# Optimization experiments

Hardware: AMD Instinct MI355X
Metric: run time of the kernel (lower is better)

## Reference

```python
import jax, jax.numpy as jnp
import numpy as np

N_NODES = 50000
N_EDGES = 800000
IN_C = 128
HID = 128
OUT_C = 64
N_GRAPHS = 256


def setup_inputs() -> dict:
    key = jax.random.key(0)
    ks = jax.random.split(key, 12)
    x = jax.random.normal(ks[0], (N_NODES, IN_C), dtype=jnp.float32)
    edge_index = jax.random.randint(ks[1], (2, N_EDGES), 0, N_NODES, dtype=jnp.int32)
    batch = jnp.sort(jax.random.randint(ks[2], (N_NODES,), 0, N_GRAPHS, dtype=jnp.int32))
    def lin(k, fan_in, fan_out):
        bound = 1.0 / np.sqrt(fan_in)
        kw, kb = jax.random.split(k)
        W = jax.random.uniform(kw, (fan_in, fan_out), minval=-bound, maxval=bound, dtype=jnp.float32)
        b = jax.random.uniform(kb, (fan_out,), minval=-bound, maxval=bound, dtype=jnp.float32)
        return W, b
    W1a, b1a = lin(ks[3], IN_C, HID)
    W1b, b1b = lin(ks[4], HID, HID)
    W2a, b2a = lin(ks[5], HID, HID)
    W2b, b2b = lin(ks[6], HID, HID)
    Wl, bl = lin(ks[7], HID, OUT_C)
    return {"x": x, "edge_index": edge_index, "batch": batch,
            "W1a": W1a, "b1a": b1a, "W1b": W1b, "b1b": b1b,
            "W2a": W2a, "b2a": b2a, "W2b": W2b, "b2b": b2b,
            "Wl": Wl, "bl": bl}


def gin_conv(x, edge_index, Wa, ba, Wb, bb):
    # GINConv with eps=0: h_i = MLP(x_i + sum_{j->i} x_j)
    src, dst = edge_index[0], edge_index[1]
    agg = jax.ops.segment_sum(x[src], dst, num_segments=x.shape[0])  # [N, d]
    h = x + agg
    h = jax.nn.relu(h @ Wa + ba) @ Wb + bb
    return h


def reference(x, edge_index, batch, W1a, b1a, W1b, b1b, W2a, b2a, W2b, b2b, Wl, bl):
    h = gin_conv(x, edge_index, W1a, b1a, W1b, b1b)
    h = gin_conv(h, edge_index, W2a, b2a, W2b, b2b)
    # global mean pool over graphs in the batch
    sums = jax.ops.segment_sum(h, batch, num_segments=N_GRAPHS)          # [G, HID]
    cnts = jax.ops.segment_sum(jnp.ones((h.shape[0],), h.dtype), batch, num_segments=N_GRAPHS)
    pooled = sums / jnp.maximum(cnts, 1.0)[:, None]
    return pooled @ Wl + bl  # [G, OUT_C]
```

## Files before the change

kernel.cpp:

```cpp
#include <hip/hip_runtime.h>

constexpr int N  = 50000;
constexpr int E  = 800000;
constexpr int C  = 128;
constexpr int G  = 256;
constexpr int OC = 64;
constexpr int D  = 64;

constexpr int TB = (E / 4 + 255) / 256;
constexpr int WB = 256;
constexpr int XB = (N * C / 8 + 255) / 256;

typedef __attribute__((ext_vector_type(8))) short short8;
typedef __attribute__((ext_vector_type(4))) float f32x4;
typedef __attribute__((ext_vector_type(2))) float f32x2;

__device__ __forceinline__ unsigned int au(float f) { return __float_as_uint(f); }

__device__ __forceinline__ unsigned short f2bf(float f) {
    unsigned int u = au(f);
    u += 0x7fffu + ((u >> 16) & 1u);
    return (unsigned short)(u >> 16);
}
__device__ __forceinline__ unsigned int pack_bf16(float lo, float hi) {
    return ((au(hi) + 0x8000u) & 0xFFFF0000u) | ((au(lo) + 0x8000u) >> 16);
}

__device__ __forceinline__ void acc16(f32x2* a, uint4 v) {
    a[0] += __builtin_amdgcn_cvt_pk_f32_fp8((int)v.x, false);
    a[1] += __builtin_amdgcn_cvt_pk_f32_fp8((int)v.x, true);
    a[2] += __builtin_amdgcn_cvt_pk_f32_fp8((int)v.y, false);
    a[3] += __builtin_amdgcn_cvt_pk_f32_fp8((int)v.y, true);
    a[4] += __builtin_amdgcn_cvt_pk_f32_fp8((int)v.z, false);
    a[5] += __builtin_amdgcn_cvt_pk_f32_fp8((int)v.z, true);
    a[6] += __builtin_amdgcn_cvt_pk_f32_fp8((int)v.w, false);
    a[7] += __builtin_amdgcn_cvt_pk_f32_fp8((int)v.w, true);
}
__device__ __forceinline__ void set16(f32x2* a, uint4 v) {
    a[0] = __builtin_amdgcn_cvt_pk_f32_fp8((int)v.x, false);
    a[1] = __builtin_amdgcn_cvt_pk_f32_fp8((int)v.x, true);
    a[2] = __builtin_amdgcn_cvt_pk_f32_fp8((int)v.y, false);
    a[3] = __builtin_amdgcn_cvt_pk_f32_fp8((int)v.y, true);
    a[4] = __builtin_amdgcn_cvt_pk_f32_fp8((int)v.z, false);
    a[5] = __builtin_amdgcn_cvt_pk_f32_fp8((int)v.z, true);
    a[6] = __builtin_amdgcn_cvt_pk_f32_fp8((int)v.w, false);
    a[7] = __builtin_amdgcn_cvt_pk_f32_fp8((int)v.w, true);
}


__global__ __launch_bounds__(256) void build_prep_kernel(const int* __restrict__ src,
                                                         const int* __restrict__ dst,
                                                         int* __restrict__ cursor,
                                                         unsigned short* __restrict__ ell,
                                                         const float* __restrict__ W1a,
                                                         const float* __restrict__ W1b,
                                                         const float* __restrict__ W2a,
                                                         const float* __restrict__ W2b,
                                                         const float* __restrict__ x,
                                                         unsigned short* __restrict__ wt,
                                                         unsigned int* __restrict__ x8) {
    int b = blockIdx.x;
    if (b < TB) {
        int t = b * 256 + threadIdx.x;
        int e0 = t * 4;
        if (e0 + 4 <= E) {
            int4 d4 = ((const int4*)dst)[t];
            int4 s4 = ((const int4*)src)[t];
            int p0 = atomicAdd(&cursor[d4.x], 1);
            int p1 = atomicAdd(&cursor[d4.y], 1);
            int p2 = atomicAdd(&cursor[d4.z], 1);
            int p3 = atomicAdd(&cursor[d4.w], 1);
            if (p0 < D) ell[(size_t)p0 * N + d4.x] = (unsigned short)s4.x;
            if (p1 < D) ell[(size_t)p1 * N + d4.y] = (unsigned short)s4.y;
            if (p2 < D) ell[(size_t)p2 * N + d4.z] = (unsigned short)s4.z;
            if (p3 < D) ell[(size_t)p3 * N + d4.w] = (unsigned short)s4.w;
        } else {
            for (int e = e0; e < E; ++e) {
                int d = dst[e];
                int p = atomicAdd(&cursor[d], 1);
                if (p < D) ell[(size_t)p * N + d] = (unsigned short)src[e];
            }
        }
    } else if (b < TB + WB) {
        const float* Ws[4] = {W1a, W1b, W2a, W2b};
        int idx = (b - TB) * 256 + threadIdx.x;
        int which = idx >> 14;
        int el    = idx & 16383;
        int n = el >> 7, k = el & 127;
        wt[idx] = f2bf(Ws[which][k * 128 + n]);
    } else {
        int idx = (b - TB - WB) * 256 + threadIdx.x;
        const float4* x4 = (const float4*)x;
        float4 v0 = x4[idx * 2];
        float4 v1 = x4[idx * 2 + 1];
        unsigned int lo = 0, hi = 0;
        lo = (unsigned int)__builtin_amdgcn_cvt_pk_fp8_f32(v0.x, v0.y, (int)lo, false);
        lo = (unsigned int)__builtin_amdgcn_cvt_pk_fp8_f32(v0.z, v0.w, (int)lo, true);
        hi = (unsigned int)__builtin_amdgcn_cvt_pk_fp8_f32(v1.x, v1.y, (int)hi, false);
        hi = (unsigned int)__builtin_amdgcn_cvt_pk_fp8_f32(v1.z, v1.w, (int)hi, true);
        ((uint2*)x8)[idx] = make_uint2(lo, hi);
    }
}


__global__ __launch_bounds__(256) void aggregate_kernel(const unsigned char* __restrict__ Fg,
                                                        const int* __restrict__ deg,
                                                        const unsigned short* __restrict__ ell,
                                                        unsigned short* __restrict__ Y) {
    int grp = threadIdx.x >> 3;
    int l   = threadIdx.x & 7;
    int n = blockIdx.x * 32 + grp;
    if (n >= N) return;
    const uint4* F16 = (const uint4*)Fg;
    f32x2 a[8];
    int dg = min(deg[n], D);
    const unsigned short* ecol = ell + n;
    set16(a, F16[(size_t)n * 8 + l]);
    int j = 0;
    if (dg >= 8) {
        int i0 = ecol[0];
        int i1 = ecol[(size_t)1 * N];
        int i2 = ecol[(size_t)2 * N];
        int i3 = ecol[(size_t)3 * N];
        int i4 = ecol[(size_t)4 * N];
        int i5 = ecol[(size_t)5 * N];
        int i6 = ecol[(size_t)6 * N];
        int i7 = ecol[(size_t)7 * N];
        uint4 v0 = F16[(size_t)i0 * 8 + l];
        uint4 v1 = F16[(size_t)i1 * 8 + l];
        uint4 v2 = F16[(size_t)i2 * 8 + l];
        uint4 v3 = F16[(size_t)i3 * 8 + l];
        uint4 v4 = F16[(size_t)i4 * 8 + l];
        uint4 v5 = F16[(size_t)i5 * 8 + l];
        uint4 v6 = F16[(size_t)i6 * 8 + l];
        uint4 v7 = F16[(size_t)i7 * 8 + l];
        for (j = 8; j + 8 <= dg; j += 8) {
            int t0 = ecol[(size_t)(j + 0) * N];
            int t1 = ecol[(size_t)(j + 1) * N];
            int t2 = ecol[(size_t)(j + 2) * N];
            int t3 = ecol[(size_t)(j + 3) * N];
            int t4 = ecol[(size_t)(j + 4) * N];
            int t5 = ecol[(size_t)(j + 5) * N];
            int t6 = ecol[(size_t)(j + 6) * N];
            int t7 = ecol[(size_t)(j + 7) * N];
            uint4 w0 = F16[(size_t)t0 * 8 + l];
            uint4 w1 = F16[(size_t)t1 * 8 + l];
            uint4 w2 = F16[(size_t)t2 * 8 + l];
            uint4 w3 = F16[(size_t)t3 * 8 + l];
            uint4 w4 = F16[(size_t)t4 * 8 + l];
            uint4 w5 = F16[(size_t)t5 * 8 + l];
            uint4 w6 = F16[(size_t)t6 * 8 + l];
            uint4 w7 = F16[(size_t)t7 * 8 + l];
            acc16(a, v0); acc16(a, v1); acc16(a, v2); acc16(a, v3);
            acc16(a, v4); acc16(a, v5); acc16(a, v6); acc16(a, v7);
            v0 = w0; v1 = w1; v2 = w2; v3 = w3;
            v4 = w4; v5 = w5; v6 = w6; v7 = w7;
        }
        acc16(a, v0); acc16(a, v1); acc16(a, v2); acc16(a, v3);
        acc16(a, v4); acc16(a, v5); acc16(a, v6); acc16(a, v7);
    }
    for (; j < dg; ++j) {
        uint4 v = F16[(size_t)ecol[(size_t)j * N] * 8 + l];
        acc16(a, v);
    }
    uint4 o0, o1;
    o0.x = pack_bf16(a[0].x, a[0].y); o0.y = pack_bf16(a[1].x, a[1].y);
    o0.z = pack_bf16(a[2].x, a[2].y); o0.w = pack_bf16(a[3].x, a[3].y);
    o1.x = pack_bf16(a[4].x, a[4].y); o1.y = pack_bf16(a[5].x, a[5].y);
    o1.z = pack_bf16(a[6].x, a[6].y); o1.w = pack_bf16(a[7].x, a[7].y);
    uint4* yp = (uint4*)(Y + (size_t)n * 128 + l * 16);
    yp[0] = o0;
    yp[1] = o1;
}


__global__ __launch_bounds__(256) void mlp_kernel(const unsigned short* __restrict__ Xg,
                                                  const unsigned short* __restrict__ WaT,
                                                  const float* __restrict__ ba,
                                                  const unsigned short* __restrict__ WbT,
                                                  const float* __restrict__ bb,
                                                  unsigned char* __restrict__ Hg8,
                                                  unsigned short* __restrict__ Hgb,
                                                  int outFp8) {
    constexpr int LD = 136;
    __shared__ short Xl[64 * LD];
    __shared__ short Wl[128 * LD];
    int tid  = threadIdx.x;
    int lane = tid & 63;
    int wave = tid >> 6;
    int row0 = blockIdx.x * 64;

    const short8* Xg8 = (const short8*)(Xg + (size_t)row0 * 128);
#pragma unroll
    for (int i = tid; i < 1024; i += 256) {
        int r = i >> 4, c = i & 15;
        *((short8*)(Xl + r * LD) + c) = Xg8[i];
    }
    const short8* Wa8 = (const short8*)WaT;
#pragma unroll
    for (int i = tid; i < 2048; i += 256) {
        int r = i >> 4, c = i & 15;
        *((short8*)(Wl + r * LD) + c) = Wa8[i];
    }

    int mw = wave >> 1, nw = wave & 1;
    int lid = lane & 15, quad = lane >> 4;

    f32x4 acc[2][4];
#pragma unroll
    for (int nt = 0; nt < 4; ++nt) {
        float b = ba[nw * 64 + nt * 16 + lid];
        acc[0][nt] = (f32x4){b, b, b, b};
        acc[1][nt] = (f32x4){b, b, b, b};
    }
    __syncthreads();

#pragma unroll
    for (int ks = 0; ks < 4; ++ks) {
        short8 a0 = *(const short8*)(Xl + (mw * 32 + lid) * LD + ks * 32 + quad * 8);
        short8 a1 = *(const short8*)(Xl + (mw * 32 + 16 + lid) * LD + ks * 32 + quad * 8);
#pragma unroll
        for (int nt = 0; nt < 4; ++nt) {
            short8 bf = *(const short8*)(Wl + (nw * 64 + nt * 16 + lid) * LD + ks * 32 + quad * 8);
            acc[0][nt] = __builtin_amdgcn_mfma_f32_16x16x32_bf16(a0, bf, acc[0][nt], 0, 0, 0);
            acc[1][nt] = __builtin_amdgcn_mfma_f32_16x16x32_bf16(a1, bf, acc[1][nt], 0, 0, 0);
        }
    }
    __syncthreads();

#pragma unroll
    for (int mt = 0; mt < 2; ++mt) {
#pragma unroll
        for (int nt = 0; nt < 4; ++nt) {
            int mbase = mw * 32 + mt * 16 + quad * 4;
            int n = nw * 64 + nt * 16 + lid;
            f32x4 v = acc[mt][nt];
#pragma unroll
            for (int r = 0; r < 4; ++r)
                Xl[(mbase + r) * LD + n] = (short)f2bf(fmaxf(v[r], 0.f));
        }
    }
    const short8* Wb8 = (const short8*)WbT;
#pragma unroll
    for (int i = tid; i < 2048; i += 256) {
        int r = i >> 4, c = i & 15;
        *((short8*)(Wl + r * LD) + c) = Wb8[i];
    }
    f32x4 acc2[2][4];
#pragma unroll
    for (int nt = 0; nt < 4; ++nt) {
        float b = bb[nw * 64 + nt * 16 + lid];
        acc2[0][nt] = (f32x4){b, b, b, b};
        acc2[1][nt] = (f32x4){b, b, b, b};
    }
    __syncthreads();

#pragma unroll
    for (int ks = 0; ks < 4; ++ks) {
        short8 a0 = *(const short8*)(Xl + (mw * 32 + lid) * LD + ks * 32 + quad * 8);
        short8 a1 = *(const short8*)(Xl + (mw * 32 + 16 + lid) * LD + ks * 32 + quad * 8);
#pragma unroll
        for (int nt = 0; nt < 4; ++nt) {
            short8 bf = *(const short8*)(Wl + (nw * 64 + nt * 16 + lid) * LD + ks * 32 + quad * 8);
            acc2[0][nt] = __builtin_amdgcn_mfma_f32_16x16x32_bf16(a0, bf, acc2[0][nt], 0, 0, 0);
            acc2[1][nt] = __builtin_amdgcn_mfma_f32_16x16x32_bf16(a1, bf, acc2[1][nt], 0, 0, 0);
        }
    }

#pragma unroll
    for (int mt = 0; mt < 2; ++mt) {
#pragma unroll
        for (int nt = 0; nt < 4; ++nt) {
            int mbase = row0 + mw * 32 + mt * 16 + quad * 4;
            int n = nw * 64 + nt * 16 + lid;
            f32x4 v = acc2[mt][nt];
            if (outFp8) {
#pragma unroll
                for (int r = 0; r < 4; ++r) {
                    int row = mbase + r;
                    if (row < N) {
                        unsigned int p = (unsigned int)__builtin_amdgcn_cvt_pk_fp8_f32(v[r], 0.f, 0, false);
                        Hg8[(size_t)row * 128 + n] = (unsigned char)(p & 0xFF);
                    }
                }
            } else {
#pragma unroll
                for (int r = 0; r < 4; ++r) {
                    int row = mbase + r;
                    if (row < N) Hgb[(size_t)row * 128 + n] = f2bf(v[r]);
                }
            }
        }
    }
}


__global__ __launch_bounds__(256) void pool_partial_kernel(const unsigned short* __restrict__ H,
                                                           const int* __restrict__ batch,
                                                           float* __restrict__ gsum,
                                                           int* __restrict__ gcnt) {
    int tid = threadIdx.x;
    int w = tid >> 6;
    int l = tid & 63;
    int r0 = blockIdx.x * 64 + w * 16;
    if (r0 >= N) return;
    int rend = min(r0 + 16, N);
    const unsigned int* H2 = (const unsigned int*)H;
    int curg = batch[r0];
    int runstart = r0;
    float a0 = 0.f, a1 = 0.f;
    for (int r = r0; r < rend; ++r) {
        int g = batch[r];
        if (g != curg) {
            atomicAdd(&gsum[curg * C + 2 * l], a0);
            atomicAdd(&gsum[curg * C + 2 * l + 1], a1);
            if (l == 0) atomicAdd(&gcnt[curg], r - runstart);
            curg = g; runstart = r; a0 = 0.f; a1 = 0.f;
        }
        unsigned int v = H2[(size_t)r * 64 + l];
        a0 += __uint_as_float((v & 0xffffu) << 16);
        a1 += __uint_as_float(v & 0xffff0000u);
    }
    atomicAdd(&gsum[curg * C + 2 * l], a0);
    atomicAdd(&gsum[curg * C + 2 * l + 1], a1);
    if (l == 0) atomicAdd(&gcnt[curg], rend - runstart);
}


__global__ __launch_bounds__(64) void head_kernel(const float* __restrict__ gsum,
                                                  const int* __restrict__ gcnt,
                                                  const float* __restrict__ Wl,
                                                  const float* __restrict__ bl,
                                                  float* __restrict__ out) {
    int g = blockIdx.x;
    int t = threadIdx.x;
    __shared__ float pooled[C];
    float inv = 1.0f / (float)max(gcnt[g], 1);
    pooled[t]      = gsum[g * C + t] * inv;
    pooled[t + 64] = gsum[g * C + 64 + t] * inv;
    __syncthreads();
    float o = bl[t];
#pragma unroll 4
    for (int k = 0; k < C; ++k) o += pooled[k] * Wl[k * OC + t];
    out[g * OC + t] = o;
}


extern "C" void kernel_launch(void* const* d_in, const int* in_sizes, int n_in,
                              void* d_out, int out_size, void* d_ws, size_t ws_size,
                              hipStream_t stream) {
    const float* x    = (const float*)d_in[0];
    const int*   ei   = (const int*)d_in[1];
    const int*   bat  = (const int*)d_in[2];
    const float* W1a  = (const float*)d_in[3];
    const float* b1a  = (const float*)d_in[4];
    const float* W1b  = (const float*)d_in[5];
    const float* b1b  = (const float*)d_in[6];
    const float* W2a  = (const float*)d_in[7];
    const float* b2a  = (const float*)d_in[8];
    const float* W2b  = (const float*)d_in[9];
    const float* b2b  = (const float*)d_in[10];
    const float* Wl   = (const float*)d_in[11];
    const float* bl   = (const float*)d_in[12];
    float*       out  = (float*)d_out;

    int*   cursor  = (int*)d_ws;
    float* gsum    = (float*)(cursor + N);
    int*   gcnt    = (int*)(gsum + G * C);
    unsigned short* ell = (unsigned short*)(gcnt + G);
    unsigned short* wt  = ell + (size_t)N * D;
    unsigned char*  x8  = (unsigned char*)(wt + 4 * 16384);
    unsigned char*  h8  = x8 + (size_t)N * 128;
    unsigned short* y   = (unsigned short*)(h8 + (size_t)N * 128);
    unsigned short* hb  = y + (size_t)(N + 64) * 128;

    const unsigned short* wt1a = wt;
    const unsigned short* wt1b = wt + 16384;
    const unsigned short* wt2a = wt + 2 * 16384;
    const unsigned short* wt2b = wt + 3 * 16384;

    const int* src = ei;
    const int* dst = ei + E;

    hipMemsetAsync(cursor, 0, (size_t)(N + G * C + G) * sizeof(int), stream);

    build_prep_kernel<<<TB + WB + XB, 256, 0, stream>>>(src, dst, cursor, ell,
                                                        W1a, W1b, W2a, W2b, x,
                                                        wt, (unsigned int*)x8);

    int ab = (N + 31) / 32;
    int mb = (N + 63) / 64;

    aggregate_kernel<<<ab, 256, 0, stream>>>(x8, cursor, ell, y);
    mlp_kernel<<<mb, 256, 0, stream>>>(y, wt1a, b1a, wt1b, b1b, h8, nullptr, 1);

    aggregate_kernel<<<ab, 256, 0, stream>>>(h8, cursor, ell, y);
    mlp_kernel<<<mb, 256, 0, stream>>>(y, wt2a, b2a, wt2b, b2b, nullptr, hb, 0);

    pool_partial_kernel<<<mb, 256, 0, stream>>>(hb, bat, gsum, gcnt);
    head_kernel<<<G, 64, 0, stream>>>(gsum, gcnt, Wl, bl, out);
}
```

Baseline: 237.1 us.

## Build ELL adjacency via two-pass bucket sort with shared-memory atomics

```diff
diff --git a/kernel.cpp b/kernel.cpp
--- a/kernel.cpp
+++ b/kernel.cpp
@@ -7,7 +7,9 @@
 constexpr int OC = 64;
 constexpr int D  = 64;
 
-constexpr int TB = (E / 4 + 255) / 256;
+constexpr int NBUCK = 196;
+constexpr int BCAP  = 5120;
+constexpr int EB = (E + 4095) / 4096;
 constexpr int WB = 256;
 constexpr int XB = (N * C / 8 + 255) / 256;
 
@@ -50,8 +52,8 @@
 
 __global__ __launch_bounds__(256) void build_prep_kernel(const int* __restrict__ src,
                                                          const int* __restrict__ dst,
-                                                         int* __restrict__ cursor,
-                                                         unsigned short* __restrict__ ell,
+                                                         int* __restrict__ bcount,
+                                                         unsigned int* __restrict__ bucketbuf,
                                                          const float* __restrict__ W1a,
                                                          const float* __restrict__ W1b,
                                                          const float* __restrict__ W2a,
@@ -60,36 +62,51 @@
                                                          unsigned short* __restrict__ wt,
                                                          unsigned int* __restrict__ x8) {
     int b = blockIdx.x;
-    if (b < TB) {
-        int t = b * 256 + threadIdx.x;
-        int e0 = t * 4;
-        if (e0 + 4 <= E) {
-            int4 d4 = ((const int4*)dst)[t];
-            int4 s4 = ((const int4*)src)[t];
-            int p0 = atomicAdd(&cursor[d4.x], 1);
-            int p1 = atomicAdd(&cursor[d4.y], 1);
-            int p2 = atomicAdd(&cursor[d4.z], 1);
-            int p3 = atomicAdd(&cursor[d4.w], 1);
-            if (p0 < D) ell[(size_t)p0 * N + d4.x] = (unsigned short)s4.x;
-            if (p1 < D) ell[(size_t)p1 * N + d4.y] = (unsigned short)s4.y;
-            if (p2 < D) ell[(size_t)p2 * N + d4.z] = (unsigned short)s4.z;
-            if (p3 < D) ell[(size_t)p3 * N + d4.w] = (unsigned short)s4.w;
-        } else {
-            for (int e = e0; e < E; ++e) {
-                int d = dst[e];
-                int p = atomicAdd(&cursor[d], 1);
-                if (p < D) ell[(size_t)p * N + d] = (unsigned short)src[e];
+    if (b < EB) {
+        __shared__ int lcount[NBUCK];
+        __shared__ int lbase[NBUCK];
+        __shared__ int lcur[NBUCK];
+        int tid = threadIdx.x;
+        for (int i = tid; i < NBUCK; i += 256) { lcount[i] = 0; lcur[i] = 0; }
+        __syncthreads();
+        int e0 = b * 4096;
+        int sv[16], dv[16];
+#pragma unroll
+        for (int i = 0; i < 16; ++i) {
+            int e = e0 + i * 256 + tid;
+            if (e < E) {
+                sv[i] = src[e];
+                dv[i] = dst[e];
+                atomicAdd(&lcount[dv[i] >> 8], 1);
+            } else {
+                dv[i] = -1;
             }
         }
-    } else if (b < TB + WB) {
+        __syncthreads();
+        if (tid < NBUCK) {
+            int c = lcount[tid];
+            lbase[tid] = (c > 0) ? atomicAdd(&bcount[tid], c) : 0;
+        }
+        __syncthreads();
+#pragma unroll
+        for (int i = 0; i < 16; ++i) {
+            if (dv[i] >= 0) {
+                int bk = dv[i] >> 8;
+                int pos = lbase[bk] + atomicAdd(&lcur[bk], 1);
+                if (pos < BCAP)
+                    bucketbuf[(size_t)bk * BCAP + pos] =
+                        ((unsigned int)sv[i] << 16) | (unsigned int)(dv[i] & 255);
+            }
+        }
+    } else if (b < EB + WB) {
         const float* Ws[4] = {W1a, W1b, W2a, W2b};
-        int idx = (b - TB) * 256 + threadIdx.x;
+        int idx = (b - EB) * 256 + threadIdx.x;
         int which = idx >> 14;
         int el    = idx & 16383;
         int n = el >> 7, k = el & 127;
         wt[idx] = f2bf(Ws[which][k * 128 + n]);
     } else {
-        int idx = (b - TB - WB) * 256 + threadIdx.x;
+        int idx = (b - EB - WB) * 256 + threadIdx.x;
         const float4* x4 = (const float4*)x;
         float4 v0 = x4[idx * 2];
         float4 v1 = x4[idx * 2 + 1];
@@ -100,6 +117,31 @@
         hi = (unsigned int)__builtin_amdgcn_cvt_pk_fp8_f32(v1.z, v1.w, (int)hi, true);
         ((uint2*)x8)[idx] = make_uint2(lo, hi);
     }
+}
+
+
+__global__ __launch_bounds__(256) void bucket_fill_kernel(const int* __restrict__ bcount,
+                                                          const unsigned int* __restrict__ bucketbuf,
+                                                          unsigned short* __restrict__ ell,
+                                                          int* __restrict__ deg) {
+    __shared__ int lcur[256];
+    int b = blockIdx.x;
+    int tid = threadIdx.x;
+    lcur[tid] = 0;
+    __syncthreads();
+    int cnt = min(bcount[b], BCAP);
+    const unsigned int* buf = bucketbuf + (size_t)b * BCAP;
+    int nbase = b << 8;
+    for (int i = tid; i < cnt; i += 256) {
+        unsigned int e = buf[i];
+        int dlow = (int)(e & 255u);
+        int s = (int)(e >> 16);
+        int p = atomicAdd(&lcur[dlow], 1);
+        if (p < D) ell[(size_t)p * N + nbase + dlow] = (unsigned short)s;
+    }
+    __syncthreads();
+    int node = nbase + tid;
+    if (node < N) deg[node] = lcur[tid];
 }
 
 
@@ -364,10 +406,12 @@
     const float* bl   = (const float*)d_in[12];
     float*       out  = (float*)d_out;
 
-    int*   cursor  = (int*)d_ws;
-    float* gsum    = (float*)(cursor + N);
+    float* gsum    = (float*)d_ws;
     int*   gcnt    = (int*)(gsum + G * C);
-    unsigned short* ell = (unsigned short*)(gcnt + G);
+    int*   bcount  = gcnt + G;
+    int*   deg     = bcount + NBUCK;
+    unsigned int* bucketbuf = (unsigned int*)(deg + N);
+    unsigned short* ell = (unsigned short*)(bucketbuf + (size_t)NBUCK * BCAP);
     unsigned short* wt  = ell + (size_t)N * D;
     unsigned char*  x8  = (unsigned char*)(wt + 4 * 16384);
     unsigned char*  h8  = x8 + (size_t)N * 128;
@@ -382,19 +426,20 @@
     const int* src = ei;
     const int* dst = ei + E;
 
-    hipMemsetAsync(cursor, 0, (size_t)(N + G * C + G) * sizeof(int), stream);
-
-    build_prep_kernel<<<TB + WB + XB, 256, 0, stream>>>(src, dst, cursor, ell,
+    hipMemsetAsync(gsum, 0, (size_t)(G * C + G + NBUCK) * sizeof(int), stream);
+
+    build_prep_kernel<<<EB + WB + XB, 256, 0, stream>>>(src, dst, bcount, bucketbuf,
                                                         W1a, W1b, W2a, W2b, x,
                                                         wt, (unsigned int*)x8);
+    bucket_fill_kernel<<<NBUCK, 256, 0, stream>>>(bcount, bucketbuf, ell, deg);
 
     int ab = (N + 31) / 32;
     int mb = (N + 63) / 64;
 
-    aggregate_kernel<<<ab, 256, 0, stream>>>(x8, cursor, ell, y);
+    aggregate_kernel<<<ab, 256, 0, stream>>>(x8, deg, ell, y);
     mlp_kernel<<<mb, 256, 0, stream>>>(y, wt1a, b1a, wt1b, b1b, h8, nullptr, 1);
 
-    aggregate_kernel<<<ab, 256, 0, stream>>>(h8, cursor, ell, y);
+    aggregate_kernel<<<ab, 256, 0, stream>>>(h8, deg, ell, y);
     mlp_kernel<<<mb, 256, 0, stream>>>(y, wt2a, b2a, wt2b, b2b, nullptr, hb, 0);
 
     pool_partial_kernel<<<mb, 256, 0, stream>>>(hb, bat, gsum, gcnt);
```

After: 221.2 us, median of 2. 6.7% less time.
